# Kernel optimization log

Hardware: AMD Instinct MI355X
Metric: run time of the kernel (lower is better)

Reference implementation:

```python
import jax, jax.numpy as jnp
import numpy as np

N = 8192
NUM_FEAT = 512
NUM_HIDDENS = 128


def _mlp_params(key, fin, fh):
    k1, k2, k3, k4 = jax.random.split(key, 4)
    s1 = 1.0 / np.sqrt(fin)
    s2 = 1.0 / np.sqrt(fh)
    W1 = jax.random.uniform(k1, (fin, fh), jnp.float32, -s1, s1)
    b1 = jax.random.uniform(k2, (fh,), jnp.float32, -s1, s1)
    W2 = jax.random.uniform(k3, (fh, fh), jnp.float32, -s2, s2)
    b2 = jax.random.uniform(k4, (fh,), jnp.float32, -s2, s2)
    return W1, b1, W2, b2


def setup_inputs() -> dict:
    key = jax.random.key(0)
    ks = jax.random.split(key, 9)
    feat = jax.random.normal(ks[0], (N, NUM_FEAT), jnp.float32)
    adj = jax.random.uniform(ks[1], (N, N), jnp.float32)
    aa = jax.random.uniform(ks[2], (N, N), jnp.float32)
    mod = jax.random.normal(ks[3], (N, N), jnp.float32)
    Wl1, bl1, Wl2, bl2 = _mlp_params(ks[4], NUM_FEAT, NUM_HIDDENS)
    Wu1, bu1, Wu2, bu2 = _mlp_params(ks[5], NUM_FEAT, NUM_HIDDENS)
    Wa1, ba1, Wa2, ba2 = _mlp_params(ks[6], NUM_FEAT, NUM_HIDDENS)
    Wm1, bm1, Wm2, bm2 = _mlp_params(ks[7], NUM_FEAT, NUM_HIDDENS)
    ws = jnp.zeros((3,), jnp.float32)  # nn.init.zeros_(weighted_sum)
    return dict(feat=feat, adj=adj, aa=aa, mod=mod,
                Wl1=Wl1, bl1=bl1, Wl2=Wl2, bl2=bl2,
                Wu1=Wu1, bu1=bu1, Wu2=Wu2, bu2=bu2,
                Wa1=Wa1, ba1=ba1, Wa2=Wa2, ba2=ba2,
                Wm1=Wm1, bm1=bm1, Wm2=Wm2, bm2=bm2,
                ws=ws)


def _latent(feat, W1, b1, W2, b2):
    h = jax.nn.relu(feat @ W1 + b1)
    return h @ W2 + b2  # [N, H]


def reference(feat, adj, aa, mod,
              Wl1, bl1, Wl2, bl2,
              Wu1, bu1, Wu2, bu2,
              Wa1, ba1, Wa2, ba2,
              Wm1, bm1, Wm2, bm2, ws):
    lat_link = _latent(feat, Wl1, bl1, Wl2, bl2)
    lat_aa = _latent(feat, Wa1, ba1, Wa2, ba2)
    lat_mod = _latent(feat, Wm1, bm1, Wm2, bm2)
    lat_unlink = _latent(feat, Wu1, bu1, Wu2, bu2)

    link_ctx = jax.nn.sigmoid(lat_link @ lat_link.T)          # [N, N]
    aa_ctx = jax.nn.sigmoid((lat_aa @ lat_aa.T) * aa)         # [N, N]
    mod_ctx = jax.nn.sigmoid((lat_mod @ lat_mod.T) * mod)     # [N, N]

    w = jax.nn.softmax(ws)  # [3]
    # cat(..., dim=2) @ w  ==  weighted sum of the three contexts
    weight_link = w[0] * link_ctx + w[1] * aa_ctx + w[2] * mod_ctx

    weight_unlink = jax.nn.sigmoid(lat_unlink @ lat_unlink.T)
    return (weight_link - weight_unlink) * adj + weight_unlink
```

## Files before the change

kernel.cpp:

```cpp
#include <hip/hip_runtime.h>


typedef __attribute__((ext_vector_type(8))) short short8;
typedef __attribute__((ext_vector_type(4))) float f32x4;

__device__ __forceinline__ unsigned short f2bf(float x) {
  union { float f; unsigned u; } v; v.f = x;
  unsigned u = v.u + 0x7FFFu + ((v.u >> 16) & 1u);
  return (unsigned short)(u >> 16);
}

__device__ __forceinline__ float sigf(float x) {
  float e = __builtin_amdgcn_exp2f(-1.4426950408889634f * x);
  return __builtin_amdgcn_rcpf(1.0f + e);
}

__device__ __forceinline__ void gload_lds16(const float* g, float* l) {
  __builtin_amdgcn_global_load_lds(
      (const __attribute__((address_space(1))) void*)g,
      (__attribute__((address_space(3))) void*)l, 16, 0, 0);
}

__global__ __launch_bounds__(256) void k_featfrag(const float* __restrict__ feat,
                                                  unsigned short* __restrict__ dst) {
  int t = blockIdx.x * 256 + threadIdx.x;
  int row = t >> 6, kc = t & 63;
  const float4* s = reinterpret_cast<const float4*>(feat + row * 512 + kc * 8);
  float4 v0 = s[0], v1 = s[1];
  short8 o;
  o[0] = f2bf(v0.x); o[1] = f2bf(v0.y); o[2] = f2bf(v0.z); o[3] = f2bf(v0.w);
  o[4] = f2bf(v1.x); o[5] = f2bf(v1.y); o[6] = f2bf(v1.z); o[7] = f2bf(v1.w);
  int mb = row >> 4, kk = kc >> 2;
  int lane = ((kc & 3) << 4) | (row & 15);
  *reinterpret_cast<short8*>(dst + ((size_t)((mb * 16 + kk) * 64 + lane)) * 8) = o;
}

__global__ __launch_bounds__(256) void k_wfrag(
    const float* __restrict__ w1_0, const float* __restrict__ w1_1,
    const float* __restrict__ w1_2, const float* __restrict__ w1_3,
    const float* __restrict__ w2_0, const float* __restrict__ w2_1,
    const float* __restrict__ w2_2, const float* __restrict__ w2_3,
    unsigned short* __restrict__ w1f, unsigned short* __restrict__ w2f) {
  int t = blockIdx.x * 256 + threadIdx.x;
  if (t < 32768) {
    int lane = t & 63, nb = (t >> 6) & 7, kk = (t >> 9) & 15, g = t >> 13;
    const float* W = g == 0 ? w1_0 : g == 1 ? w1_1 : g == 2 ? w1_2 : w1_3;
    int q = lane >> 4, r = lane & 15;
    int col = nb * 16 + r;
    short8 o;
#pragma unroll
    for (int j = 0; j < 8; ++j) o[j] = f2bf(W[(kk * 32 + q * 8 + j) * 128 + col]);
    *reinterpret_cast<short8*>(w1f + (size_t)t * 8) = o;
  } else if (t < 40960) {
    int t2 = t - 32768;
    int lane = t2 & 63, nb = (t2 >> 6) & 7, kk = (t2 >> 9) & 3, g = t2 >> 11;
    const float* W = g == 0 ? w2_0 : g == 1 ? w2_1 : g == 2 ? w2_2 : w2_3;
    int q = lane >> 4, r = lane & 15;
    int col = nb * 16 + r;
    short8 o;
#pragma unroll
    for (int j = 0; j < 8; ++j) o[j] = f2bf(W[(kk * 32 + q * 8 + j) * 128 + col]);
    *reinterpret_cast<short8*>(w2f + (size_t)t2 * 8) = o;
  }
}

__global__ __launch_bounds__(256) void k_gemm1(
    const unsigned short* __restrict__ featf, const unsigned short* __restrict__ w1f,
    const float* __restrict__ b1_0, const float* __restrict__ b1_1,
    const float* __restrict__ b1_2, const float* __restrict__ b1_3,
    unsigned short* __restrict__ hfrag) {
  int bi = blockIdx.x, g = blockIdx.y;
  int lane = threadIdx.x & 63, w = threadIdx.x >> 6;
  int wm = w >> 1, wn = w & 1;
  int q = lane >> 4, r = lane & 15;
  int mbase = 8 * bi + 4 * wm;

  f32x4 s[4][4];
#pragma unroll
  for (int mi = 0; mi < 4; ++mi)
#pragma unroll
    for (int nj = 0; nj < 4; ++nj) s[mi][nj] = (f32x4){0.f, 0.f, 0.f, 0.f};

  for (int kk = 0; kk < 16; ++kk) {
    short8 a[4], b[4];
#pragma unroll
    for (int mi = 0; mi < 4; ++mi)
      a[mi] = *reinterpret_cast<const short8*>(
          featf + ((size_t)(((mbase + mi) * 16 + kk) * 64 + lane)) * 8);
#pragma unroll
    for (int nj = 0; nj < 4; ++nj)
      b[nj] = *reinterpret_cast<const short8*>(
          w1f + ((size_t)(((g * 16 + kk) * 8 + 4 * wn + nj) * 64 + lane)) * 8);
#pragma unroll
    for (int mi = 0; mi < 4; ++mi)
#pragma unroll
      for (int nj = 0; nj < 4; ++nj)
        s[mi][nj] = __builtin_amdgcn_mfma_f32_16x16x32_bf16(a[mi], b[nj], s[mi][nj], 0, 0, 0);
  }

  const float* b1 = g == 0 ? b1_0 : g == 1 ? b1_1 : g == 2 ? b1_2 : b1_3;
#pragma unroll
  for (int nj = 0; nj < 4; ++nj) {
    int cl = 64 * wn + 16 * nj + r;
    float bias = b1[cl];
    int Cg = 128 * g + cl;
    int kkd = Cg >> 5;
    int lane2hi = ((Cg >> 3) & 3) << 4;
    int j2 = Cg & 7;
#pragma unroll
    for (int mi = 0; mi < 4; ++mi) {
#pragma unroll
      for (int v = 0; v < 4; ++v) {
        int R = 128 * bi + 64 * wm + 16 * mi + 4 * q + v;
        float val = fmaxf(s[mi][nj][v] + bias, 0.0f);
        int mb = R >> 4;
        int lane2 = lane2hi | (R & 15);
        hfrag[((size_t)((mb * 16 + kkd) * 64 + lane2)) * 8 + j2] = f2bf(val);
      }
    }
  }
}

__global__ __launch_bounds__(256) void k_gemm2(
    const unsigned short* __restrict__ hfrag, const unsigned short* __restrict__ w2f,
    const float* __restrict__ b2_0, const float* __restrict__ b2_1,
    const float* __restrict__ b2_2, const float* __restrict__ b2_3,
    unsigned short* __restrict__ latf) {
  int bi = blockIdx.x, g = blockIdx.y;
  int lane = threadIdx.x & 63, w = threadIdx.x >> 6;
  int wm = w >> 1, wn = w & 1;
  int q = lane >> 4, r = lane & 15;
  int mbase = 8 * bi + 4 * wm;

  f32x4 s[4][4];
#pragma unroll
  for (int mi = 0; mi < 4; ++mi)
#pragma unroll
    for (int nj = 0; nj < 4; ++nj) s[mi][nj] = (f32x4){0.f, 0.f, 0.f, 0.f};

#pragma unroll
  for (int kk = 0; kk < 4; ++kk) {
    short8 a[4], b[4];
#pragma unroll
    for (int mi = 0; mi < 4; ++mi)
      a[mi] = *reinterpret_cast<const short8*>(
          hfrag + ((size_t)(((mbase + mi) * 16 + 4 * g + kk) * 64 + lane)) * 8);
#pragma unroll
    for (int nj = 0; nj < 4; ++nj)
      b[nj] = *reinterpret_cast<const short8*>(
          w2f + ((size_t)(((g * 4 + kk) * 8 + 4 * wn + nj) * 64 + lane)) * 8);
#pragma unroll
    for (int mi = 0; mi < 4; ++mi)
#pragma unroll
      for (int nj = 0; nj < 4; ++nj)
        s[mi][nj] = __builtin_amdgcn_mfma_f32_16x16x32_bf16(a[mi], b[nj], s[mi][nj], 0, 0, 0);
  }

  const float* b2 = g == 0 ? b2_0 : g == 1 ? b2_1 : g == 2 ? b2_2 : b2_3;
#pragma unroll
  for (int nj = 0; nj < 4; ++nj) {
    int cl = 64 * wn + 16 * nj + r;
    float bias = b2[cl];
    int kkd = cl >> 5;
    int lane2hi = ((cl >> 3) & 3) << 4;
    int j2 = cl & 7;
#pragma unroll
    for (int mi = 0; mi < 4; ++mi) {
#pragma unroll
      for (int v = 0; v < 4; ++v) {
        int R = 128 * bi + 64 * wm + 16 * mi + 4 * q + v;
        float val = s[mi][nj][v] + bias;
        int mb = R >> 4;
        int lane2 = lane2hi | (R & 15);
        latf[((size_t)(((g * 512 + mb) * 4 + kkd) * 64 + lane2)) * 8 + j2] = f2bf(val);
      }
    }
  }
}

__global__ __launch_bounds__(512, 4) void k_ctx(
    const unsigned short* __restrict__ latf,
    const float* __restrict__ adj, const float* __restrict__ aa,
    const float* __restrict__ mod, const float* __restrict__ wsv,
    float* __restrict__ out) {
  __shared__ float smem[2][3][2048];

  int bid = blockIdx.x;
  int colstrip = bid & 7;
  int rowgrp = bid >> 3;

  int tid = threadIdx.x;
  int lane = tid & 63, w = tid >> 6;
  int q = lane >> 4, r = lane & 15;

  int mbi = rowgrp * 8 + w;
  int mbj0 = colstrip * 64;

  size_t ewoff = (size_t)(mbi * 16 + r) * 8192 + (size_t)mbj0 * 16 + 4 * q;

  float s0w = wsv[0], s1w = wsv[1], s2w = wsv[2];
  float mx = fmaxf(fmaxf(s0w, s1w), s2w);
  float e0 = __builtin_amdgcn_exp2f(1.4426950408889634f * (s0w - mx));
  float e1 = __builtin_amdgcn_exp2f(1.4426950408889634f * (s1w - mx));
  float e2 = __builtin_amdgcn_exp2f(1.4426950408889634f * (s2w - mx));
  float inv = __builtin_amdgcn_rcpf(e0 + e1 + e2);
  float w0 = e0 * inv, w1 = e1 * inv, w2 = e2 * inv;

  const size_t GS = (size_t)512 * 2048;

  short8 fi[4][4];
#pragma unroll
  for (int g = 0; g < 4; ++g)
#pragma unroll
    for (int kk = 0; kk < 4; ++kk) {
      fi[g][kk] = *reinterpret_cast<const short8*>(
          latf + GS * g + (((size_t)mbi * 4 + kk) << 9) + lane * 8);
      asm volatile("" : "+v"(fi[g][kk]));
    }

  gload_lds16(aa + ewoff, &smem[0][0][w * 256]);
  gload_lds16(mod + ewoff, &smem[0][1][w * 256]);
  gload_lds16(adj + ewoff, &smem[0][2][w * 256]);
  asm volatile("s_waitcnt vmcnt(0)" ::: "memory");
  __syncthreads();

  for (int t = 0; t < 64; ++t) {
    int buf = t & 1, nbuf = buf ^ 1;
    bool dofill = (t < 63);
    size_t ewnext = ewoff + (size_t)(t + 1) * 16;
    const unsigned short* fjb =
        latf + (((size_t)(mbj0 + t) * 4) << 9) + lane * 8;

    f32x4 sg, o4;

    {
      short8 fj0 = *reinterpret_cast<const short8*>(fjb + GS * 0);
      short8 fj1 = *reinterpret_cast<const short8*>(fjb + GS * 0 + 512);
      short8 fj2 = *reinterpret_cast<const short8*>(fjb + GS * 0 + 1024);
      short8 fj3 = *reinterpret_cast<const short8*>(fjb + GS * 0 + 1536);
      if (dofill) gload_lds16(aa + ewnext, &smem[nbuf][0][w * 256]);
      __builtin_amdgcn_sched_barrier(0);
      sg = (f32x4){0.f, 0.f, 0.f, 0.f};
      sg = __builtin_amdgcn_mfma_f32_16x16x32_bf16(fj0, fi[0][0], sg, 0, 0, 0);
      sg = __builtin_amdgcn_mfma_f32_16x16x32_bf16(fj1, fi[0][1], sg, 0, 0, 0);
      sg = __builtin_amdgcn_mfma_f32_16x16x32_bf16(fj2, fi[0][2], sg, 0, 0, 0);
      sg = __builtin_amdgcn_mfma_f32_16x16x32_bf16(fj3, fi[0][3], sg, 0, 0, 0);
#pragma unroll
      for (int v = 0; v < 4; ++v) o4[v] = w0 * sigf(sg[v]);
    }

    {
      short8 fj0 = *reinterpret_cast<const short8*>(fjb + GS * 1);
      short8 fj1 = *reinterpret_cast<const short8*>(fjb + GS * 1 + 512);
      short8 fj2 = *reinterpret_cast<const short8*>(fjb + GS * 1 + 1024);
      short8 fj3 = *reinterpret_cast<const short8*>(fjb + GS * 1 + 1536);
      if (dofill) gload_lds16(mod + ewnext, &smem[nbuf][1][w * 256]);
      __builtin_amdgcn_sched_barrier(0);
      sg = (f32x4){0.f, 0.f, 0.f, 0.f};
      sg = __builtin_amdgcn_mfma_f32_16x16x32_bf16(fj0, fi[1][0], sg, 0, 0, 0);
      sg = __builtin_amdgcn_mfma_f32_16x16x32_bf16(fj1, fi[1][1], sg, 0, 0, 0);
      sg = __builtin_amdgcn_mfma_f32_16x16x32_bf16(fj2, fi[1][2], sg, 0, 0, 0);
      sg = __builtin_amdgcn_mfma_f32_16x16x32_bf16(fj3, fi[1][3], sg, 0, 0, 0);
      f32x4 ew = *reinterpret_cast<const f32x4*>(&smem[buf][0][w * 256 + lane * 4]);
#pragma unroll
      for (int v = 0; v < 4; ++v) o4[v] += w1 * sigf(sg[v] * ew[v]);
    }

    {
      short8 fj0 = *reinterpret_cast<const short8*>(fjb + GS * 2);
      short8 fj1 = *reinterpret_cast<const short8*>(fjb + GS * 2 + 512);
      short8 fj2 = *reinterpret_cast<const short8*>(fjb + GS * 2 + 1024);
      short8 fj3 = *reinterpret_cast<const short8*>(fjb + GS * 2 + 1536);
      if (dofill) gload_lds16(adj + ewnext, &smem[nbuf][2][w * 256]);
      __builtin_amdgcn_sched_barrier(0);
      sg = (f32x4){0.f, 0.f, 0.f, 0.f};
      sg = __builtin_amdgcn_mfma_f32_16x16x32_bf16(fj0, fi[2][0], sg, 0, 0, 0);
      sg = __builtin_amdgcn_mfma_f32_16x16x32_bf16(fj1, fi[2][1], sg, 0, 0, 0);
      sg = __builtin_amdgcn_mfma_f32_16x16x32_bf16(fj2, fi[2][2], sg, 0, 0, 0);
      sg = __builtin_amdgcn_mfma_f32_16x16x32_bf16(fj3, fi[2][3], sg, 0, 0, 0);
      f32x4 ew = *reinterpret_cast<const f32x4*>(&smem[buf][1][w * 256 + lane * 4]);
#pragma unroll
      for (int v = 0; v < 4; ++v) o4[v] += w2 * sigf(sg[v] * ew[v]);
    }

    {
      short8 fj0 = *reinterpret_cast<const short8*>(fjb + GS * 3);
      short8 fj1 = *reinterpret_cast<const short8*>(fjb + GS * 3 + 512);
      short8 fj2 = *reinterpret_cast<const short8*>(fjb + GS * 3 + 1024);
      short8 fj3 = *reinterpret_cast<const short8*>(fjb + GS * 3 + 1536);
      sg = (f32x4){0.f, 0.f, 0.f, 0.f};
      sg = __builtin_amdgcn_mfma_f32_16x16x32_bf16(fj0, fi[3][0], sg, 0, 0, 0);
      sg = __builtin_amdgcn_mfma_f32_16x16x32_bf16(fj1, fi[3][1], sg, 0, 0, 0);
      sg = __builtin_amdgcn_mfma_f32_16x16x32_bf16(fj2, fi[3][2], sg, 0, 0, 0);
      sg = __builtin_amdgcn_mfma_f32_16x16x32_bf16(fj3, fi[3][3], sg, 0, 0, 0);
      f32x4 ew = *reinterpret_cast<const f32x4*>(&smem[buf][2][w * 256 + lane * 4]);
      f32x4 res;
#pragma unroll
      for (int v = 0; v < 4; ++v) {
        float u = sigf(sg[v]);
        res[v] = ew[v] * (o4[v] - u) + u;
      }
      *reinterpret_cast<f32x4*>(out + ewoff + (size_t)t * 16) = res;
    }

    asm volatile("s_waitcnt vmcnt(0)" ::: "memory");
    __syncthreads();
  }
}

extern "C" void kernel_launch(void* const* d_in, const int* in_sizes, int n_in,
                              void* d_out, int out_size, void* d_ws, size_t ws_size,
                              hipStream_t stream) {
  const float* feat = (const float*)d_in[0];
  const float* adj  = (const float*)d_in[1];
  const float* aa   = (const float*)d_in[2];
  const float* mod  = (const float*)d_in[3];
  const float* W1g[4] = {(const float*)d_in[4], (const float*)d_in[12],
                         (const float*)d_in[16], (const float*)d_in[8]};
  const float* b1g[4] = {(const float*)d_in[5], (const float*)d_in[13],
                         (const float*)d_in[17], (const float*)d_in[9]};
  const float* W2g[4] = {(const float*)d_in[6], (const float*)d_in[14],
                         (const float*)d_in[18], (const float*)d_in[10]};
  const float* b2g[4] = {(const float*)d_in[7], (const float*)d_in[15],
                         (const float*)d_in[19], (const float*)d_in[11]};
  const float* wsv = (const float*)d_in[20];
  float* out = (float*)d_out;

  unsigned short* featf = (unsigned short*)d_ws;
  unsigned short* hfrag = featf + 4194304;
  unsigned short* latf  = hfrag + 4194304;
  unsigned short* w1f   = latf + 4194304;
  unsigned short* w2f   = w1f + 262144;
  if (ws_size < 25821184) return;

  k_featfrag<<<2048, 256, 0, stream>>>(feat, featf);
  k_wfrag<<<160, 256, 0, stream>>>(W1g[0], W1g[1], W1g[2], W1g[3],
                                   W2g[0], W2g[1], W2g[2], W2g[3], w1f, w2f);
  k_gemm1<<<dim3(64, 4), 256, 0, stream>>>(featf, w1f, b1g[0], b1g[1], b1g[2], b1g[3], hfrag);
  k_gemm2<<<dim3(64, 4), 256, 0, stream>>>(hfrag, w2f, b2g[0], b2g[1], b2g[2], b2g[3], latf);
  k_ctx<<<512, 512, 0, stream>>>(latf, adj, aa, mod, wsv, out);
}
```

Baseline: 412.4 us.

## Restructure ctx kernel into per-wave pipelines without block barriers

Each wave now prefetches its own slice of aa, mod and adj into a private LDS double buffer. The per-tile `__syncthreads` is replaced by a `vmcnt(3)` wait, so the latest three prefetches stay in flight while compute proceeds. All 16 latent fragments for the tile are loaded up front, blocks shrink to 256 threads (grid of 1024), and outputs are written with nontemporal stores. The aim is to remove block-wide stalls and overlap streaming of the large elementwise inputs with MFMA and sigmoid work. The cost is more registers for the batched fragment loads. The `vmcnt` accounting also relies on stores and loads being counted together.

```diff
diff --git a/kernel.cpp b/kernel.cpp
--- a/kernel.cpp
+++ b/kernel.cpp
@@ -178,12 +178,12 @@
   }
 }
 
-__global__ __launch_bounds__(512, 4) void k_ctx(
+__global__ __launch_bounds__(256, 3) void k_ctx(
     const unsigned short* __restrict__ latf,
     const float* __restrict__ adj, const float* __restrict__ aa,
     const float* __restrict__ mod, const float* __restrict__ wsv,
     float* __restrict__ out) {
-  __shared__ float smem[2][3][2048];
+  __shared__ float smem[2][3][4][256];
 
   int bid = blockIdx.x;
   int colstrip = bid & 7;
@@ -193,10 +193,10 @@
   int lane = tid & 63, w = tid >> 6;
   int q = lane >> 4, r = lane & 15;
 
-  int mbi = rowgrp * 8 + w;
+  int mbi = rowgrp * 4 + w;
   int mbj0 = colstrip * 64;
 
-  size_t ewoff = (size_t)(mbi * 16 + r) * 8192 + (size_t)mbj0 * 16 + 4 * q;
+  size_t ewoff = (size_t)(mbi * 16 + r) * 8192 + (size_t)colstrip * 1024 + 4 * q;
 
   float s0w = wsv[0], s1w = wsv[1], s2w = wsv[2];
   float mx = fmaxf(fmaxf(s0w, s1w), s2w);
@@ -218,93 +218,79 @@
       asm volatile("" : "+v"(fi[g][kk]));
     }
 
-  gload_lds16(aa + ewoff, &smem[0][0][w * 256]);
-  gload_lds16(mod + ewoff, &smem[0][1][w * 256]);
-  gload_lds16(adj + ewoff, &smem[0][2][w * 256]);
+  gload_lds16(aa + ewoff, &smem[0][0][w][0]);
+  gload_lds16(mod + ewoff, &smem[0][1][w][0]);
+  gload_lds16(adj + ewoff, &smem[0][2][w][0]);
   asm volatile("s_waitcnt vmcnt(0)" ::: "memory");
-  __syncthreads();
 
   for (int t = 0; t < 64; ++t) {
     int buf = t & 1, nbuf = buf ^ 1;
-    bool dofill = (t < 63);
-    size_t ewnext = ewoff + (size_t)(t + 1) * 16;
     const unsigned short* fjb =
         latf + (((size_t)(mbj0 + t) * 4) << 9) + lane * 8;
 
+    short8 fj[4][4];
+#pragma unroll
+    for (int g = 0; g < 4; ++g)
+#pragma unroll
+      for (int kk = 0; kk < 4; ++kk)
+        fj[g][kk] = *reinterpret_cast<const short8*>(fjb + GS * g + 512 * kk);
+
+    __builtin_amdgcn_sched_barrier(0);
+    {
+      size_t ewnext = ewoff + (size_t)(t < 63 ? t + 1 : t) * 16;
+      gload_lds16(aa + ewnext, &smem[nbuf][0][w][0]);
+      gload_lds16(mod + ewnext, &smem[nbuf][1][w][0]);
+      gload_lds16(adj + ewnext, &smem[nbuf][2][w][0]);
+    }
+    asm volatile("s_waitcnt vmcnt(3)" ::: "memory");
+
     f32x4 sg, o4;
 
+    sg = (f32x4){0.f, 0.f, 0.f, 0.f};
+    sg = __builtin_amdgcn_mfma_f32_16x16x32_bf16(fj[0][0], fi[0][0], sg, 0, 0, 0);
+    sg = __builtin_amdgcn_mfma_f32_16x16x32_bf16(fj[0][1], fi[0][1], sg, 0, 0, 0);
+    sg = __builtin_amdgcn_mfma_f32_16x16x32_bf16(fj[0][2], fi[0][2], sg, 0, 0, 0);
+    sg = __builtin_amdgcn_mfma_f32_16x16x32_bf16(fj[0][3], fi[0][3], sg, 0, 0, 0);
+#pragma unroll
+    for (int v = 0; v < 4; ++v) o4[v] = w0 * sigf(sg[v]);
+
+    sg = (f32x4){0.f, 0.f, 0.f, 0.f};
+    sg = __builtin_amdgcn_mfma_f32_16x16x32_bf16(fj[1][0], fi[1][0], sg, 0, 0, 0);
+    sg = __builtin_amdgcn_mfma_f32_16x16x32_bf16(fj[1][1], fi[1][1], sg, 0, 0, 0);
+    sg = __builtin_amdgcn_mfma_f32_16x16x32_bf16(fj[1][2], fi[1][2], sg, 0, 0, 0);
+    sg = __builtin_amdgcn_mfma_f32_16x16x32_bf16(fj[1][3], fi[1][3], sg, 0, 0, 0);
     {
-      short8 fj0 = *reinterpret_cast<const short8*>(fjb + GS * 0);
-      short8 fj1 = *reinterpret_cast<const short8*>(fjb + GS * 0 + 512);
-      short8 fj2 = *reinterpret_cast<const short8*>(fjb + GS * 0 + 1024);
-      short8 fj3 = *reinterpret_cast<const short8*>(fjb + GS * 0 + 1536);
-      if (dofill) gload_lds16(aa + ewnext, &smem[nbuf][0][w * 256]);
-      __builtin_amdgcn_sched_barrier(0);
-      sg = (f32x4){0.f, 0.f, 0.f, 0.f};
-      sg = __builtin_amdgcn_mfma_f32_16x16x32_bf16(fj0, fi[0][0], sg, 0, 0, 0);
-      sg = __builtin_amdgcn_mfma_f32_16x16x32_bf16(fj1, fi[0][1], sg, 0, 0, 0);
-      sg = __builtin_amdgcn_mfma_f32_16x16x32_bf16(fj2, fi[0][2], sg, 0, 0, 0);
-      sg = __builtin_amdgcn_mfma_f32_16x16x32_bf16(fj3, fi[0][3], sg, 0, 0, 0);
-#pragma unroll
-      for (int v = 0; v < 4; ++v) o4[v] = w0 * sigf(sg[v]);
-    }
-
+      f32x4 ew = *reinterpret_cast<const f32x4*>(&smem[buf][0][w][lane * 4]);
+#pragma unroll
+      for (int v = 0; v < 4; ++v) o4[v] += w1 * sigf(sg[v] * ew[v]);
+    }
+
+    sg = (f32x4){0.f, 0.f, 0.f, 0.f};
+    sg = __builtin_amdgcn_mfma_f32_16x16x32_bf16(fj[2][0], fi[2][0], sg, 0, 0, 0);
+    sg = __builtin_amdgcn_mfma_f32_16x16x32_bf16(fj[2][1], fi[2][1], sg, 0, 0, 0);
+    sg = __builtin_amdgcn_mfma_f32_16x16x32_bf16(fj[2][2], fi[2][2], sg, 0, 0, 0);
+    sg = __builtin_amdgcn_mfma_f32_16x16x32_bf16(fj[2][3], fi[2][3], sg, 0, 0, 0);
     {
-      short8 fj0 = *reinterpret_cast<const short8*>(fjb + GS * 1);
-      short8 fj1 = *reinterpret_cast<const short8*>(fjb + GS * 1 + 512);
-      short8 fj2 = *reinterpret_cast<const short8*>(fjb + GS * 1 + 1024);
-      short8 fj3 = *reinterpret_cast<const short8*>(fjb + GS * 1 + 1536);
-      if (dofill) gload_lds16(mod + ewnext, &smem[nbuf][1][w * 256]);
-      __builtin_amdgcn_sched_barrier(0);
-      sg = (f32x4){0.f, 0.f, 0.f, 0.f};
-      sg = __builtin_amdgcn_mfma_f32_16x16x32_bf16(fj0, fi[1][0], sg, 0, 0, 0);
-      sg = __builtin_amdgcn_mfma_f32_16x16x32_bf16(fj1, fi[1][1], sg, 0, 0, 0);
-      sg = __builtin_amdgcn_mfma_f32_16x16x32_bf16(fj2, fi[1][2], sg, 0, 0, 0);
-      sg = __builtin_amdgcn_mfma_f32_16x16x32_bf16(fj3, fi[1][3], sg, 0, 0, 0);
-      f32x4 ew = *reinterpret_cast<const f32x4*>(&smem[buf][0][w * 256 + lane * 4]);
-#pragma unroll
-      for (int v = 0; v < 4; ++v) o4[v] += w1 * sigf(sg[v] * ew[v]);
-    }
-
+      f32x4 ew = *reinterpret_cast<const f32x4*>(&smem[buf][1][w][lane * 4]);
+#pragma unroll
+      for (int v = 0; v < 4; ++v) o4[v] += w2 * sigf(sg[v] * ew[v]);
+    }
+
+    sg = (f32x4){0.f, 0.f, 0.f, 0.f};
+    sg = __builtin_amdgcn_mfma_f32_16x16x32_bf16(fj[3][0], fi[3][0], sg, 0, 0, 0);
+    sg = __builtin_amdgcn_mfma_f32_16x16x32_bf16(fj[3][1], fi[3][1], sg, 0, 0, 0);
+    sg = __builtin_amdgcn_mfma_f32_16x16x32_bf16(fj[3][2], fi[3][2], sg, 0, 0, 0);
+    sg = __builtin_amdgcn_mfma_f32_16x16x32_bf16(fj[3][3], fi[3][3], sg, 0, 0, 0);
     {
-      short8 fj0 = *reinterpret_cast<const short8*>(fjb + GS * 2);
-      short8 fj1 = *reinterpret_cast<const short8*>(fjb + GS * 2 + 512);
-      short8 fj2 = *reinterpret_cast<const short8*>(fjb + GS * 2 + 1024);
-      short8 fj3 = *reinterpret_cast<const short8*>(fjb + GS * 2 + 1536);
-      if (dofill) gload_lds16(adj + ewnext, &smem[nbuf][2][w * 256]);
-      __builtin_amdgcn_sched_barrier(0);
-      sg = (f32x4){0.f, 0.f, 0.f, 0.f};
-      sg = __builtin_amdgcn_mfma_f32_16x16x32_bf16(fj0, fi[2][0], sg, 0, 0, 0);
-      sg = __builtin_amdgcn_mfma_f32_16x16x32_bf16(fj1, fi[2][1], sg, 0, 0, 0);
-      sg = __builtin_amdgcn_mfma_f32_16x16x32_bf16(fj2, fi[2][2], sg, 0, 0, 0);
-      sg = __builtin_amdgcn_mfma_f32_16x16x32_bf16(fj3, fi[2][3], sg, 0, 0, 0);
-      f32x4 ew = *reinterpret_cast<const f32x4*>(&smem[buf][1][w * 256 + lane * 4]);
-#pragma unroll
-      for (int v = 0; v < 4; ++v) o4[v] += w2 * sigf(sg[v] * ew[v]);
-    }
-
-    {
-      short8 fj0 = *reinterpret_cast<const short8*>(fjb + GS * 3);
-      short8 fj1 = *reinterpret_cast<const short8*>(fjb + GS * 3 + 512);
-      short8 fj2 = *reinterpret_cast<const short8*>(fjb + GS * 3 + 1024);
-      short8 fj3 = *reinterpret_cast<const short8*>(fjb + GS * 3 + 1536);
-      sg = (f32x4){0.f, 0.f, 0.f, 0.f};
-      sg = __builtin_amdgcn_mfma_f32_16x16x32_bf16(fj0, fi[3][0], sg, 0, 0, 0);
-      sg = __builtin_amdgcn_mfma_f32_16x16x32_bf16(fj1, fi[3][1], sg, 0, 0, 0);
-      sg = __builtin_amdgcn_mfma_f32_16x16x32_bf16(fj2, fi[3][2], sg, 0, 0, 0);
-      sg = __builtin_amdgcn_mfma_f32_16x16x32_bf16(fj3, fi[3][3], sg, 0, 0, 0);
-      f32x4 ew = *reinterpret_cast<const f32x4*>(&smem[buf][2][w * 256 + lane * 4]);
+      f32x4 ew = *reinterpret_cast<const f32x4*>(&smem[buf][2][w][lane * 4]);
       f32x4 res;
 #pragma unroll
       for (int v = 0; v < 4; ++v) {
         float u = sigf(sg[v]);
         res[v] = ew[v] * (o4[v] - u) + u;
       }
-      *reinterpret_cast<f32x4*>(out + ewoff + (size_t)t * 16) = res;
-    }
-
-    asm volatile("s_waitcnt vmcnt(0)" ::: "memory");
-    __syncthreads();
+      __builtin_nontemporal_store(res, reinterpret_cast<f32x4*>(out + ewoff + (size_t)t * 16));
+    }
   }
 }
 
@@ -338,5 +324,5 @@
                                    W2g[0], W2g[1], W2g[2], W2g[3], w1f, w2f);
   k_gemm1<<<dim3(64, 4), 256, 0, stream>>>(featf, w1f, b1g[0], b1g[1], b1g[2], b1g[3], hfrag);
   k_gemm2<<<dim3(64, 4), 256, 0, stream>>>(hfrag, w2f, b2g[0], b2g[1], b2g[2], b2g[3], latf);
-  k_ctx<<<512, 512, 0, stream>>>(latf, adj, aa, mod, wsv, out);
-}
+  k_ctx<<<1024, 256, 0, stream>>>(latf, adj, aa, mod, wsv, out);
+}
```

Result: slower. 448.9 us (+8.8%).
